# Performance work log

Hardware: AMD Instinct MI355X
Metric: run time of the kernel (lower is better)

## Reference

```python
import jax, jax.numpy as jnp
import numpy as np

N_NODES = 100000
N_EDGES = 1600000
IN_CH = 128
HEADS = 4
HEAD_DIM = 16  # out_channels // heads = 64 // 4
EPS = 1e-8
NEG_SLOPE = 0.2


def setup_inputs() -> dict:
    key = jax.random.key(0)
    k1, k2, k3, k4, k5 = jax.random.split(key, 5)
    x = jax.random.normal(k1, (N_NODES, IN_CH), dtype=jnp.float32)
    edge_index = jax.random.randint(k2, (2, N_EDGES), 0, N_NODES, dtype=jnp.int64)
    edge_weight = jax.random.uniform(k3, (N_EDGES,), dtype=jnp.float32)
    # Linear(in_channels, heads*head_dim, bias=False): weight [out, in]
    W = jax.random.normal(k4, (HEADS * HEAD_DIM, IN_CH), dtype=jnp.float32) * 0.05
    a = jax.random.normal(k5, (1, HEADS, 2 * HEAD_DIM), dtype=jnp.float32) * 0.1
    return {"x": x, "edge_index": edge_index, "edge_weight": edge_weight, "W": W, "a": a}


def reference(x, edge_index, edge_weight, W, a):
    num_nodes = x.shape[0]
    h = (x @ W.T).reshape(num_nodes, HEADS, HEAD_DIM)  # [N, H, D]
    src, dst = edge_index[0], edge_index[1]
    h_src = h[src]  # [E, H, D]
    h_dst = h[dst]  # [E, H, D]
    # a * concat(h_src, h_dst) summed over last dim == split-dot (avoids concat)
    a_src = a[..., :HEAD_DIM]  # [1, H, D]
    a_dst = a[..., HEAD_DIM:]  # [1, H, D]
    attention = jnp.sum(a_src * h_src + a_dst * h_dst, axis=-1)  # [E, H]
    attention = jax.nn.leaky_relu(attention, negative_slope=NEG_SLOPE)
    attention = attention * edge_weight[:, None]
    attention = jnp.exp(attention)
    att_sum = jax.ops.segment_sum(attention, dst, num_segments=num_nodes)  # [N, H]
    attention = attention / (att_sum[dst] + EPS)  # [E, H]
    # dropout is identity in eval mode
    weighted = h_src * attention[:, :, None]  # [E, H, D]
    out = jax.ops.segment_sum(weighted, dst, num_segments=num_nodes)  # [N, H, D]
    return out.reshape(num_nodes, HEADS * HEAD_DIM)
```

## Files before the change

kernel.cpp:

```cpp
#include <hip/hip_runtime.h>
#include <math.h>

#define N_NODES 100000
#define N_EDGES 1600000
#define IN_CH 128
#define HEADS 4
#define HEAD_DIM 16
#define OUT_CH 64
#define NEG_SLOPE 0.2f
#define EPS 1e-8f

#define NBUCK 391
#define NBLK1 512
#define CHUNK (N_EDGES / NBLK1)
#define CAPG 4608
#define CAP CAPG

typedef _Float16 f16x8 __attribute__((ext_vector_type(8)));
typedef _Float16 f16x4 __attribute__((ext_vector_type(4)));
typedef float    f32x4 __attribute__((ext_vector_type(4)));

#define SWZ(b) ((b) ^ ((((b) >> 8) & 7) << 4))

__global__ __launch_bounds__(128) void prep16_kernel(
    const float* __restrict__ W, const float* __restrict__ a,
    _Float16* __restrict__ Wh, int* __restrict__ gcur)
{
    int k = threadIdx.x;
    for (int i = k; i < NBUCK + 1; i += 128) gcur[i] = 0;
#pragma unroll
    for (int r = 0; r < 64; r++)
        Wh[r * IN_CH + k] = (_Float16)W[r * IN_CH + k];
#pragma unroll
    for (int hd = 0; hd < 4; hd++) {
        float ss = 0.f, dd = 0.f;
#pragma unroll
        for (int c = 0; c < 16; c++) {
            float wv = W[(hd * 16 + c) * IN_CH + k];
            ss += a[hd * 32 + c] * wv;
            dd += a[hd * 32 + 16 + c] * wv;
        }
        Wh[(64 + hd) * IN_CH + k] = (_Float16)ss;
        Wh[(68 + hd) * IN_CH + k] = (_Float16)dd;
    }
}

__device__ inline f16x8 cvt8(const float* p) {
    float4 lo = ((const float4*)p)[0];
    float4 hi = ((const float4*)p)[1];
    f16x8 f;
    f[0] = (_Float16)lo.x; f[1] = (_Float16)lo.y;
    f[2] = (_Float16)lo.z; f[3] = (_Float16)lo.w;
    f[4] = (_Float16)hi.x; f[5] = (_Float16)hi.y;
    f[6] = (_Float16)hi.z; f[7] = (_Float16)hi.w;
    return f;
}

__global__ __launch_bounds__(512, 6) void gemm_alpha_kernel(
    const float* __restrict__ x,
    const _Float16* __restrict__ Wh,
    _Float16* __restrict__ h,
    float* __restrict__ alpha_src,
    float* __restrict__ alpha_dst)
{
    __shared__ _Float16 whs[72 * 128];
    __shared__ _Float16 hst[128 * 72];

    const int wv = threadIdx.x >> 6;
    const int lane = threadIdx.x & 63;
    const int col = lane & 15;
    const int quad = lane >> 4;

    for (int c = threadIdx.x; c < 1152; c += 512) {
        int b = c << 4;
        *(f16x8*)((char*)whs + SWZ(b)) = *(const f16x8*)((const char*)Wh + b);
    }
    __syncthreads();

    const int node_base = blockIdx.x * 128 + wv * 16;
    int row_node = node_base + col;
    int rn = row_node < N_NODES ? row_node : N_NODES - 1;
    const float* xrow = x + (long long)rn * IN_CH;

    f16x8 afrag[4];
#pragma unroll
    for (int ks = 0; ks < 4; ks++)
        afrag[ks] = cvt8(xrow + ks * 32 + quad * 8);

    f32x4 acc[5];
#pragma unroll
    for (int nt = 0; nt < 5; nt++) {
        f32x4 z = {0.f, 0.f, 0.f, 0.f};
        acc[nt] = z;
    }

#pragma unroll
    for (int ks = 0; ks < 4; ks++) {
#pragma unroll
        for (int nt = 0; nt < 5; nt++) {
            int r = (nt < 4) ? nt * 16 + col : 64 + (col & 7);
            int b = (r << 8) + (ks << 6) + (quad << 4);
            f16x8 bf = *(const f16x8*)((const char*)whs + SWZ(b));
            if (nt == 4 && col >= 8) {
                f16x8 z = {};
                bf = z;
            }
            acc[nt] = __builtin_amdgcn_mfma_f32_16x16x32_f16(
                afrag[ks], bf, acc[nt], 0, 0, 0);
        }
    }

#pragma unroll
    for (int r = 0; r < 4; r++) {
        int nl = wv * 16 + quad * 4 + r;
#pragma unroll
        for (int nt = 0; nt < 4; nt++)
            hst[nl * 72 + nt * 16 + col] = (_Float16)acc[nt][r];
        int node = node_base + quad * 4 + r;
        if (node < N_NODES) {
            if (col < 4)      alpha_src[node * HEADS + col]     = acc[4][r];
            else if (col < 8) alpha_dst[node * HEADS + col - 4] = acc[4][r];
        }
    }

    __syncthreads();
    const int bnode = blockIdx.x * 128;
    const int nrem = N_NODES - bnode;
    const int climit = (nrem < 128 ? nrem : 128) << 3;
    for (int i = threadIdx.x; i < 1024; i += 512) {
        if (i < climit) {
            int node = i >> 3, ch8 = i & 7;
            *(f16x8*)(h + (long long)(bnode + node) * OUT_CH + ch8 * 8) =
                *(const f16x8*)&hst[node * 72 + ch8 * 8];
        }
    }
}

__global__ __launch_bounds__(512) void fused_count_scatter_kernel(
    const int* __restrict__ ei, const float* __restrict__ ew,
    int* __restrict__ gcur,
    unsigned long long* __restrict__ tmp)
{
    __shared__ int cnt[NBUCK];
    __shared__ int dbuf[CHUNK];
    for (int j = threadIdx.x; j < NBUCK; j += 512) cnt[j] = 0;
    __syncthreads();
    const int base = blockIdx.x * CHUNK;
    for (int i = threadIdx.x; i < CHUNK; i += 512) {
        int d = ei[N_EDGES + base + i];
        dbuf[i] = d;
        atomicAdd(&cnt[d >> 8], 1);
    }
    __syncthreads();
    for (int j = threadIdx.x; j < NBUCK; j += 512) {
        int c = cnt[j];
        int b = (c > 0) ? atomicAdd(&gcur[j], c) : 0;
        cnt[j] = j * CAPG + b;
    }
    __syncthreads();
    for (int i = threadIdx.x; i < CHUNK; i += 512) {
        int e = base + i;
        int d = dbuf[i];
        int s = ei[e];
        float w = ew[e];
        int pos = atomicAdd(&cnt[d >> 8], 1);
        unsigned long long pk = ((unsigned long long)__float_as_uint(w) << 32)
                              | ((unsigned)(d & 255) << 17) | (unsigned)s;
        tmp[pos] = pk;
    }
}

__global__ __launch_bounds__(512) void bucket_offsets_kernel(
    const int* __restrict__ gcur, int* __restrict__ bucketStart,
    int* __restrict__ ptr)
{
    __shared__ int part[512];
    const int t = threadIdx.x;
    int v = (t < NBUCK) ? gcur[t] : 0;
    part[t] = v;
    __syncthreads();
    for (int off = 1; off < 512; off <<= 1) {
        int x = (t >= off) ? part[t - off] : 0;
        __syncthreads();
        part[t] += x;
        __syncthreads();
    }
    if (t < NBUCK) bucketStart[t] = part[t] - v;
    if (t == 0) { bucketStart[NBUCK] = N_EDGES; ptr[N_NODES] = N_EDGES; }
}

__global__ __launch_bounds__(512) void finalize_kernel(
    const unsigned long long* __restrict__ tmp,
    const int* __restrict__ gcur,
    const int* __restrict__ bucketStart,
    long long* __restrict__ csr, int* __restrict__ ptr)
{
    __shared__ int cnt[256];
    __shared__ int offs[256];
    __shared__ unsigned short rk[CAP];
    __shared__ unsigned long long stage[CAP];
    const int j = blockIdx.x;
    const int t = threadIdx.x;
    const int beg = bucketStart[j];
    const int len = gcur[j];
    const unsigned long long* src = tmp + (size_t)j * CAPG;

    if (t < 256) cnt[t] = 0;
    __syncthreads();

    for (int i = t; i < len; i += 512) {
        unsigned long long pk = __builtin_nontemporal_load(&src[i]);
        stage[i] = pk;
        rk[i] = (unsigned short)atomicAdd(&cnt[(int)((pk >> 17) & 255)], 1);
    }
    __syncthreads();
    int v = (t < 256) ? cnt[t] : 0;
    for (int off = 1; off < 256; off <<= 1) {
        int x = (t < 256 && t >= off) ? cnt[t - off] : 0;
        __syncthreads();
        if (t < 256) cnt[t] += x;
        __syncthreads();
    }
    if (t < 256) {
        int excl = cnt[t] - v;
        int node = j * 256 + t;
        if (node < N_NODES) ptr[node] = beg + excl;
        offs[t] = excl;
    }
    __syncthreads();
    for (int i = t; i < len; i += 512) {
        unsigned long long pk = stage[i];
        int dloc = (int)((pk >> 17) & 255);
        int pos = offs[dloc] + (int)rk[i];
        unsigned long long vv = (pk & 0xFFFFFFFF00000000ull) | (pk & 0x1FFFFull);
        ((unsigned long long*)csr)[beg + pos] = vv;
    }
}

__global__ __launch_bounds__(256) void aggregate_kernel(
    const int* __restrict__ ptr,
    const int2* __restrict__ csr,
    const float4* __restrict__ alpha_src4,
    const float4* __restrict__ alpha_dst4,
    const _Float16* __restrict__ h,
    float* __restrict__ out)
{
    __shared__ float4 sev[4][64];
    __shared__ int    ssc[4][64];

    const int wv = threadIdx.x >> 6;
    const int lane = threadIdx.x & 63;
    const int n = blockIdx.x * 4 + wv;
    if (n >= N_NODES) return;
    const int q = lane >> 4;
    const int cg = lane & 15;
    const int hsel = cg >> 2;

    const int beg = ptr[n];
    const int end = ptr[n + 1];
    const float4 ad4 = alpha_dst4[n];

    float4 acc = make_float4(0.f, 0.f, 0.f, 0.f);
    float denom = 0.f;
    float4* sev_w = sev[wv];
    int* ssc_w = ssc[wv];

    for (int base = beg; base < end; base += 64) {
        int cnt = min(64, end - base);
        int s_l = 0;
        float4 e4 = make_float4(0.f, 0.f, 0.f, 0.f);
        if (lane < cnt) {
            int2 pr = csr[base + lane];
            s_l = pr.x;
            float w = __int_as_float(pr.y);
            float4 as = alpha_src4[s_l];
            float t0 = as.x + ad4.x; t0 = (t0 > 0.f ? t0 : NEG_SLOPE * t0) * w;
            float t1 = as.y + ad4.y; t1 = (t1 > 0.f ? t1 : NEG_SLOPE * t1) * w;
            float t2 = as.z + ad4.z; t2 = (t2 > 0.f ? t2 : NEG_SLOPE * t2) * w;
            float t3 = as.w + ad4.w; t3 = (t3 > 0.f ? t3 : NEG_SLOPE * t3) * w;
            e4 = make_float4(__expf(t0), __expf(t1), __expf(t2), __expf(t3));
        }
        sev_w[lane] = e4;
        ssc_w[lane] = s_l;

        int iters = (cnt + 3) >> 2;
        for (int j0 = 0; j0 < iters; j0 += 2) {
            int idx0 = j0 * 4 + q;
            int idx1 = idx0 + 4;
            int s0 = ssc_w[idx0];
            int s1 = ssc_w[idx1];
            float ev0 = ((const float*)&sev_w[idx0])[hsel];
            float ev1 = ((const float*)&sev_w[idx1])[hsel];
            f16x4 h0 = *(const f16x4*)(h + s0 * OUT_CH + cg * 4);
            f16x4 h1 = *(const f16x4*)(h + s1 * OUT_CH + cg * 4);
            acc.x += ev0 * (float)h0[0] + ev1 * (float)h1[0];
            acc.y += ev0 * (float)h0[1] + ev1 * (float)h1[1];
            acc.z += ev0 * (float)h0[2] + ev1 * (float)h1[2];
            acc.w += ev0 * (float)h0[3] + ev1 * (float)h1[3];
            denom += ev0 + ev1;
        }
    }

    denom += __shfl_xor(denom, 16);
    denom += __shfl_xor(denom, 32);
    acc.x += __shfl_xor(acc.x, 16);  acc.x += __shfl_xor(acc.x, 32);
    acc.y += __shfl_xor(acc.y, 16);  acc.y += __shfl_xor(acc.y, 32);
    acc.z += __shfl_xor(acc.z, 16);  acc.z += __shfl_xor(acc.z, 32);
    acc.w += __shfl_xor(acc.w, 16);  acc.w += __shfl_xor(acc.w, 32);

    if (lane < 16) {
        float inv = 1.f / (denom + EPS);
        float4 r = make_float4(acc.x * inv, acc.y * inv, acc.z * inv, acc.w * inv);
        ((float4*)(out + (long long)n * OUT_CH))[cg] = r;
    }
}

extern "C" void kernel_launch(void* const* d_in, const int* in_sizes, int n_in,
                              void* d_out, int out_size, void* d_ws, size_t ws_size,
                              hipStream_t stream) {
    const float* x  = (const float*)d_in[0];
    const int*   ei = (const int*)d_in[1];
    const float* ew = (const float*)d_in[2];
    const float* W  = (const float*)d_in[3];
    const float* a  = (const float*)d_in[4];
    float* out = (float*)d_out;

    char* p = (char*)d_ws;
    _Float16* h      = (_Float16*)p; p += (size_t)N_NODES * OUT_CH * 2;
    float* alpha_src = (float*)p;  p += (size_t)N_NODES * HEADS * 4;
    float* alpha_dst = (float*)p;  p += (size_t)N_NODES * HEADS * 4;
    _Float16* Wh     = (_Float16*)p; p += (size_t)72 * IN_CH * 2;
    int*   gcur      = (int*)p;    p += (size_t)392 * 4;
    int*   bstart    = (int*)p;    p += (size_t)392 * 4;
    int*   ptr       = (int*)p;    p += (size_t)(N_NODES + 4) * 4;
    unsigned long long* tmp = (unsigned long long*)p;
    p += (size_t)NBUCK * CAPG * 8;
    long long* csr   = (long long*)p;

    prep16_kernel<<<1, 128, 0, stream>>>(W, a, Wh, gcur);
    fused_count_scatter_kernel<<<NBLK1, 512, 0, stream>>>(ei, ew, gcur, tmp);
    bucket_offsets_kernel<<<1, 512, 0, stream>>>(gcur, bstart, ptr);
    gemm_alpha_kernel<<<(N_NODES + 127) / 128, 512, 0, stream>>>(x, Wh, h, alpha_src, alpha_dst);
    finalize_kernel<<<NBUCK, 512, 0, stream>>>(tmp, gcur, bstart, csr, ptr);
    aggregate_kernel<<<(N_NODES + 3) / 4, 256, 0, stream>>>(
        ptr, (const int2*)csr, (const float4*)alpha_src, (const float4*)alpha_dst, h, out);
}
```

Measured before the change: 205.3 us.

## Merge edge bucketing and GEMM into one heterogeneous launch; fold prep and scan

The edge count/scatter blocks and the node GEMM blocks now run in a single grid that branches on block index, so the two independent phases can overlap on the GPU. The weight conversion and attention-vector folding from the prep kernel are recomputed in every GEMM block, and the bucket prefix scan moves into each finalize block. A memset replaces the counter reset. This removes three launches and their serialization, at the cost of redundant per-block W/a work and a larger shared-memory footprint for the scatter blocks.

```diff
diff --git a/kernel.cpp b/kernel.cpp
--- a/kernel.cpp
+++ b/kernel.cpp
@@ -15,35 +15,14 @@
 #define CHUNK (N_EDGES / NBLK1)
 #define CAPG 4608
 #define CAP CAPG
+#define GEMM_BLOCKS ((N_NODES + 127) / 128)
+#define FAT_BLOCKS (NBLK1 + GEMM_BLOCKS)
 
 typedef _Float16 f16x8 __attribute__((ext_vector_type(8)));
 typedef _Float16 f16x4 __attribute__((ext_vector_type(4)));
 typedef float    f32x4 __attribute__((ext_vector_type(4)));
 
 #define SWZ(b) ((b) ^ ((((b) >> 8) & 7) << 4))
-
-__global__ __launch_bounds__(128) void prep16_kernel(
-    const float* __restrict__ W, const float* __restrict__ a,
-    _Float16* __restrict__ Wh, int* __restrict__ gcur)
-{
-    int k = threadIdx.x;
-    for (int i = k; i < NBUCK + 1; i += 128) gcur[i] = 0;
-#pragma unroll
-    for (int r = 0; r < 64; r++)
-        Wh[r * IN_CH + k] = (_Float16)W[r * IN_CH + k];
-#pragma unroll
-    for (int hd = 0; hd < 4; hd++) {
-        float ss = 0.f, dd = 0.f;
-#pragma unroll
-        for (int c = 0; c < 16; c++) {
-            float wv = W[(hd * 16 + c) * IN_CH + k];
-            ss += a[hd * 32 + c] * wv;
-            dd += a[hd * 32 + 16 + c] * wv;
-        }
-        Wh[(64 + hd) * IN_CH + k] = (_Float16)ss;
-        Wh[(68 + hd) * IN_CH + k] = (_Float16)dd;
-    }
-}
 
 __device__ inline f16x8 cvt8(const float* p) {
     float4 lo = ((const float4*)p)[0];
@@ -56,157 +35,165 @@
     return f;
 }
 
-__global__ __launch_bounds__(512, 6) void gemm_alpha_kernel(
+__global__ __launch_bounds__(512, 6) void gemm_scatter_kernel(
     const float* __restrict__ x,
-    const _Float16* __restrict__ Wh,
+    const float* __restrict__ W,
+    const float* __restrict__ a,
+    const int* __restrict__ ei,
+    const float* __restrict__ ew,
+    int* __restrict__ gcur,
+    unsigned long long* __restrict__ tmp,
     _Float16* __restrict__ h,
     float* __restrict__ alpha_src,
     float* __restrict__ alpha_dst)
 {
-    __shared__ _Float16 whs[72 * 128];
-    __shared__ _Float16 hst[128 * 72];
-
-    const int wv = threadIdx.x >> 6;
-    const int lane = threadIdx.x & 63;
-    const int col = lane & 15;
-    const int quad = lane >> 4;
-
-    for (int c = threadIdx.x; c < 1152; c += 512) {
-        int b = c << 4;
-        *(f16x8*)((char*)whs + SWZ(b)) = *(const f16x8*)((const char*)Wh + b);
-    }
-    __syncthreads();
-
-    const int node_base = blockIdx.x * 128 + wv * 16;
-    int row_node = node_base + col;
-    int rn = row_node < N_NODES ? row_node : N_NODES - 1;
-    const float* xrow = x + (long long)rn * IN_CH;
-
-    f16x8 afrag[4];
-#pragma unroll
-    for (int ks = 0; ks < 4; ks++)
-        afrag[ks] = cvt8(xrow + ks * 32 + quad * 8);
-
-    f32x4 acc[5];
-#pragma unroll
-    for (int nt = 0; nt < 5; nt++) {
-        f32x4 z = {0.f, 0.f, 0.f, 0.f};
-        acc[nt] = z;
-    }
-
-#pragma unroll
-    for (int ks = 0; ks < 4; ks++) {
+    __shared__ __align__(16) char smem[36864];
+
+    if (blockIdx.x < NBLK1) {
+        int* cnt  = (int*)smem;
+        int* dbuf = (int*)(smem + 1664);
+        for (int j = threadIdx.x; j < NBUCK; j += 512) cnt[j] = 0;
+        __syncthreads();
+        const int base = blockIdx.x * CHUNK;
+        for (int i = threadIdx.x; i < CHUNK; i += 512) {
+            int d = ei[N_EDGES + base + i];
+            dbuf[i] = d;
+            atomicAdd(&cnt[d >> 8], 1);
+        }
+        __syncthreads();
+        for (int j = threadIdx.x; j < NBUCK; j += 512) {
+            int c = cnt[j];
+            int b = (c > 0) ? atomicAdd(&gcur[j], c) : 0;
+            cnt[j] = j * CAPG + b;
+        }
+        __syncthreads();
+        for (int i = threadIdx.x; i < CHUNK; i += 512) {
+            int e = base + i;
+            int d = dbuf[i];
+            int s = ei[e];
+            float w = ew[e];
+            int pos = atomicAdd(&cnt[d >> 8], 1);
+            unsigned long long pk = ((unsigned long long)__float_as_uint(w) << 32)
+                                  | ((unsigned)(d & 255) << 17) | (unsigned)s;
+            tmp[pos] = pk;
+        }
+    } else {
+        _Float16* whs = (_Float16*)smem;
+        _Float16* hst = (_Float16*)(smem + 18432);
+
+        const int gb = blockIdx.x - NBLK1;
+        const int wv = threadIdx.x >> 6;
+        const int lane = threadIdx.x & 63;
+        const int col = lane & 15;
+        const int quad = lane >> 4;
+
+        for (int i = threadIdx.x; i < 1024; i += 512) {
+            int row = i >> 4, koff = (i & 15) << 3;
+            int b = (row << 8) + (koff << 1);
+            *(f16x8*)((char*)whs + SWZ(b)) = cvt8(W + row * IN_CH + koff);
+        }
+        for (int i = threadIdx.x; i < 1024; i += 512) {
+            int r8 = i >> 7, k = i & 127;
+            int hd = r8 & 3, half = r8 >> 2;
+            const float* av = a + hd * 32 + half * 16;
+            const float* wb = W + hd * 16 * IN_CH + k;
+            float s = 0.f;
+#pragma unroll
+            for (int c = 0; c < 16; c++)
+                s += av[c] * wb[c * IN_CH];
+            int b = ((64 + r8) << 8) + (k << 1);
+            *(_Float16*)((char*)whs + SWZ(b)) = (_Float16)s;
+        }
+        __syncthreads();
+
+        const int node_base = gb * 128 + wv * 16;
+        int row_node = node_base + col;
+        int rn = row_node < N_NODES ? row_node : N_NODES - 1;
+        const float* xrow = x + (long long)rn * IN_CH;
+
+        f16x8 afrag[4];
+#pragma unroll
+        for (int ks = 0; ks < 4; ks++)
+            afrag[ks] = cvt8(xrow + ks * 32 + quad * 8);
+
+        f32x4 acc[5];
 #pragma unroll
         for (int nt = 0; nt < 5; nt++) {
-            int r = (nt < 4) ? nt * 16 + col : 64 + (col & 7);
-            int b = (r << 8) + (ks << 6) + (quad << 4);
-            f16x8 bf = *(const f16x8*)((const char*)whs + SWZ(b));
-            if (nt == 4 && col >= 8) {
-                f16x8 z = {};
-                bf = z;
+            f32x4 z = {0.f, 0.f, 0.f, 0.f};
+            acc[nt] = z;
+        }
+
+#pragma unroll
+        for (int ks = 0; ks < 4; ks++) {
+#pragma unroll
+            for (int nt = 0; nt < 5; nt++) {
+                int r = (nt < 4) ? nt * 16 + col : 64 + (col & 7);
+                int b = (r << 8) + (ks << 6) + (quad << 4);
+                f16x8 bf = *(const f16x8*)((const char*)whs + SWZ(b));
+                if (nt == 4 && col >= 8) {
+                    f16x8 z = {};
+                    bf = z;
+                }
+                acc[nt] = __builtin_amdgcn_mfma_f32_16x16x32_f16(
+                    afrag[ks], bf, acc[nt], 0, 0, 0);
             }
-            acc[nt] = __builtin_amdgcn_mfma_f32_16x16x32_f16(
-                afrag[ks], bf, acc[nt], 0, 0, 0);
-        }
-    }
-
-#pragma unroll
-    for (int r = 0; r < 4; r++) {
-        int nl = wv * 16 + quad * 4 + r;
-#pragma unroll
-        for (int nt = 0; nt < 4; nt++)
-            hst[nl * 72 + nt * 16 + col] = (_Float16)acc[nt][r];
-        int node = node_base + quad * 4 + r;
-        if (node < N_NODES) {
-            if (col < 4)      alpha_src[node * HEADS + col]     = acc[4][r];
-            else if (col < 8) alpha_dst[node * HEADS + col - 4] = acc[4][r];
-        }
-    }
-
-    __syncthreads();
-    const int bnode = blockIdx.x * 128;
-    const int nrem = N_NODES - bnode;
-    const int climit = (nrem < 128 ? nrem : 128) << 3;
-    for (int i = threadIdx.x; i < 1024; i += 512) {
-        if (i < climit) {
-            int node = i >> 3, ch8 = i & 7;
-            *(f16x8*)(h + (long long)(bnode + node) * OUT_CH + ch8 * 8) =
-                *(const f16x8*)&hst[node * 72 + ch8 * 8];
-        }
-    }
-}
-
-__global__ __launch_bounds__(512) void fused_count_scatter_kernel(
-    const int* __restrict__ ei, const float* __restrict__ ew,
-    int* __restrict__ gcur,
-    unsigned long long* __restrict__ tmp)
-{
-    __shared__ int cnt[NBUCK];
-    __shared__ int dbuf[CHUNK];
-    for (int j = threadIdx.x; j < NBUCK; j += 512) cnt[j] = 0;
-    __syncthreads();
-    const int base = blockIdx.x * CHUNK;
-    for (int i = threadIdx.x; i < CHUNK; i += 512) {
-        int d = ei[N_EDGES + base + i];
-        dbuf[i] = d;
-        atomicAdd(&cnt[d >> 8], 1);
-    }
-    __syncthreads();
-    for (int j = threadIdx.x; j < NBUCK; j += 512) {
-        int c = cnt[j];
-        int b = (c > 0) ? atomicAdd(&gcur[j], c) : 0;
-        cnt[j] = j * CAPG + b;
-    }
-    __syncthreads();
-    for (int i = threadIdx.x; i < CHUNK; i += 512) {
-        int e = base + i;
-        int d = dbuf[i];
-        int s = ei[e];
-        float w = ew[e];
-        int pos = atomicAdd(&cnt[d >> 8], 1);
-        unsigned long long pk = ((unsigned long long)__float_as_uint(w) << 32)
-                              | ((unsigned)(d & 255) << 17) | (unsigned)s;
-        tmp[pos] = pk;
-    }
-}
-
-__global__ __launch_bounds__(512) void bucket_offsets_kernel(
-    const int* __restrict__ gcur, int* __restrict__ bucketStart,
-    int* __restrict__ ptr)
-{
-    __shared__ int part[512];
-    const int t = threadIdx.x;
-    int v = (t < NBUCK) ? gcur[t] : 0;
-    part[t] = v;
-    __syncthreads();
-    for (int off = 1; off < 512; off <<= 1) {
-        int x = (t >= off) ? part[t - off] : 0;
-        __syncthreads();
-        part[t] += x;
-        __syncthreads();
-    }
-    if (t < NBUCK) bucketStart[t] = part[t] - v;
-    if (t == 0) { bucketStart[NBUCK] = N_EDGES; ptr[N_NODES] = N_EDGES; }
+        }
+
+#pragma unroll
+        for (int r = 0; r < 4; r++) {
+            int nl = wv * 16 + quad * 4 + r;
+#pragma unroll
+            for (int nt = 0; nt < 4; nt++)
+                hst[nl * 72 + nt * 16 + col] = (_Float16)acc[nt][r];
+            int node = node_base + quad * 4 + r;
+            if (node < N_NODES) {
+                if (col < 4)      alpha_src[node * HEADS + col]     = acc[4][r];
+                else if (col < 8) alpha_dst[node * HEADS + col - 4] = acc[4][r];
+            }
+        }
+
+        __syncthreads();
+        const int bnode = gb * 128;
+        const int nrem = N_NODES - bnode;
+        const int climit = (nrem < 128 ? nrem : 128) << 3;
+        for (int i = threadIdx.x; i < 1024; i += 512) {
+            if (i < climit) {
+                int node = i >> 3, ch8 = i & 7;
+                *(f16x8*)(h + (long long)(bnode + node) * OUT_CH + ch8 * 8) =
+                    *(const f16x8*)&hst[node * 72 + ch8 * 8];
+            }
+        }
+    }
 }
 
 __global__ __launch_bounds__(512) void finalize_kernel(
     const unsigned long long* __restrict__ tmp,
     const int* __restrict__ gcur,
-    const int* __restrict__ bucketStart,
     long long* __restrict__ csr, int* __restrict__ ptr)
 {
     __shared__ int cnt[256];
     __shared__ int offs[256];
+    __shared__ int scanbuf[512];
     __shared__ unsigned short rk[CAP];
     __shared__ unsigned long long stage[CAP];
     const int j = blockIdx.x;
     const int t = threadIdx.x;
-    const int beg = bucketStart[j];
-    const int len = gcur[j];
-    const unsigned long long* src = tmp + (size_t)j * CAPG;
-
+
+    int gv = (t < NBUCK) ? gcur[t] : 0;
+    scanbuf[t] = gv;
     if (t < 256) cnt[t] = 0;
     __syncthreads();
+    for (int off = 1; off < 512; off <<= 1) {
+        int xx = (t >= off) ? scanbuf[t - off] : 0;
+        __syncthreads();
+        scanbuf[t] += xx;
+        __syncthreads();
+    }
+    const int incl = scanbuf[j];
+    const int beg  = (j > 0) ? scanbuf[j - 1] : 0;
+    const int len  = incl - beg;
+    if (j == 0 && t == 0) ptr[N_NODES] = N_EDGES;
+    const unsigned long long* src = tmp + (size_t)j * CAPG;
 
     for (int i = t; i < len; i += 512) {
         unsigned long long pk = __builtin_nontemporal_load(&src[i]);
@@ -216,9 +203,9 @@
     __syncthreads();
     int v = (t < 256) ? cnt[t] : 0;
     for (int off = 1; off < 256; off <<= 1) {
-        int x = (t < 256 && t >= off) ? cnt[t - off] : 0;
-        __syncthreads();
-        if (t < 256) cnt[t] += x;
+        int xx = (t < 256 && t >= off) ? cnt[t - off] : 0;
+        __syncthreads();
+        if (t < 256) cnt[t] += xx;
         __syncthreads();
     }
     if (t < 256) {
@@ -329,19 +316,17 @@
     _Float16* h      = (_Float16*)p; p += (size_t)N_NODES * OUT_CH * 2;
     float* alpha_src = (float*)p;  p += (size_t)N_NODES * HEADS * 4;
     float* alpha_dst = (float*)p;  p += (size_t)N_NODES * HEADS * 4;
-    _Float16* Wh     = (_Float16*)p; p += (size_t)72 * IN_CH * 2;
-    int*   gcur      = (int*)p;    p += (size_t)392 * 4;
-    int*   bstart    = (int*)p;    p += (size_t)392 * 4;
+    int*   gcur      = (int*)p;    p += (size_t)400 * 4;
     int*   ptr       = (int*)p;    p += (size_t)(N_NODES + 4) * 4;
     unsigned long long* tmp = (unsigned long long*)p;
     p += (size_t)NBUCK * CAPG * 8;
     long long* csr   = (long long*)p;
 
-    prep16_kernel<<<1, 128, 0, stream>>>(W, a, Wh, gcur);
-    fused_count_scatter_kernel<<<NBLK1, 512, 0, stream>>>(ei, ew, gcur, tmp);
-    bucket_offsets_kernel<<<1, 512, 0, stream>>>(gcur, bstart, ptr);
-    gemm_alpha_kernel<<<(N_NODES + 127) / 128, 512, 0, stream>>>(x, Wh, h, alpha_src, alpha_dst);
-    finalize_kernel<<<NBUCK, 512, 0, stream>>>(tmp, gcur, bstart, csr, ptr);
+    hipMemsetAsync(gcur, 0, 400 * sizeof(int), stream);
+
+    gemm_scatter_kernel<<<FAT_BLOCKS, 512, 0, stream>>>(
+        x, W, a, ei, ew, gcur, tmp, h, alpha_src, alpha_dst);
+    finalize_kernel<<<NBUCK, 512, 0, stream>>>(tmp, gcur, csr, ptr);
     aggregate_kernel<<<(N_NODES + 3) / 4, 256, 0, stream>>>(
         ptr, (const int2*)csr, (const float4*)alpha_src, (const float4*)alpha_dst, h, out);
 }
```

After: 193.0 us. 1.06x faster.
